# Kernel optimization log

Hardware: AMD Instinct MI355X
Metric: run time of the kernel (lower is better)

## Reference

```python
import math
import jax, jax.numpy as jnp
import numpy as np

OLEN = 512
RATIO = 0.5
DROP_P = 0.2


def _gat(x, src, dst, W, a_s, a_d, b):
    """PyG GATConv (heads=1, concat=True, add_self_loops=True, neg_slope=0.2)."""
    n = x.shape[0]
    loops = jnp.arange(n, dtype=src.dtype)
    s = jnp.concatenate([src, loops])  # [E+N] source nodes
    d = jnp.concatenate([dst, loops])  # [E+N] destination nodes
    h = x @ W                           # [N, H]
    alpha_s = h @ a_s                   # [N]
    alpha_d = h @ a_d                   # [N]
    e = jax.nn.leaky_relu(alpha_s[s] + alpha_d[d], 0.2)  # [E+N]
    # segment softmax over destination neighborhoods
    m = jax.ops.segment_max(e, d, num_segments=n)
    ee = jnp.exp(e - m[d])
    denom = jax.ops.segment_sum(ee, d, num_segments=n)
    alpha = ee / denom[d]
    out = jax.ops.segment_sum(alpha[:, None] * h[s], d, num_segments=n)
    return out + b


def _forward(x, src, dst, W1, a_src1, a_dst1, b1, W2, a_src2, a_dst2, b2,
             W3, a_src3, a_dst3, b3, W_rel, W_root, b_pool):
    N, E = x.shape[0], src.shape[0]
    key = jax.random.key(42)
    h = x
    for i, (W, a_s, a_d, b) in enumerate([(W1, a_src1, a_dst1, b1),
                                          (W2, a_src2, a_dst2, b2),
                                          (W3, a_src3, a_dst3, b3)]):
        h = jax.nn.relu(_gat(h, src, dst, W, a_s, a_d, b))
        keep = jax.random.bernoulli(jax.random.fold_in(key, i), 1.0 - DROP_P, h.shape)
        h = jnp.where(keep, h / (1.0 - DROP_P), 0.0)  # F.dropout(training=True)

    # SAGPooling(GraphConv score, ratio=0.5, tanh) repeated until n <= 512.
    # Node counts are static per iteration (k = ceil(0.5*n)); edge arrays keep
    # fixed size E with a validity mask (edges dropped when an endpoint is pooled away).
    cur_src, cur_dst = src, dst
    emask = jnp.ones((E,), dtype=h.dtype)
    n = N
    while True:
        agg = jax.ops.segment_sum(h[cur_src] * emask[:, None], cur_dst, num_segments=n)
        score = (agg @ W_rel + h @ W_root + b_pool)[:, 0]  # GraphConv(d->1), aggr='add'
        score = jnp.tanh(score)
        k = math.ceil(RATIO * n)
        top_vals, perm = jax.lax.top_k(score, k)
        h = h[perm] * top_vals[:, None]
        inv = jnp.full((n,), -1, dtype=cur_src.dtype).at[perm].set(
            jnp.arange(k, dtype=cur_src.dtype))
        ns, nd = inv[cur_src], inv[cur_dst]
        valid = (ns >= 0) & (nd >= 0)
        emask = emask * valid.astype(emask.dtype)
        cur_src = jnp.where(valid, ns, 0)
        cur_dst = jnp.where(valid, nd, 0)
        n = k
        if n <= OLEN:
            break

    out = jnp.zeros((OLEN, h.shape[1]), h.dtype).at[:n].set(h)
    return out


def setup_inputs() -> dict:
    key = jax.random.key(0)
    ks = jax.random.split(key, 20)
    N, E, IDIM, HDIM = 50000, 800000, 128, 200
    inp = {
        "x": jax.random.normal(ks[0], (N, IDIM), jnp.float32),
        "src": jax.random.randint(ks[1], (E,), 0, N, jnp.int32),
        "dst": jax.random.randint(ks[2], (E,), 0, N, jnp.int32),
    }
    def w(k, shape, fan_in):
        return jax.random.normal(k, shape, jnp.float32) / np.sqrt(fan_in).astype(np.float32)
    inp["W1"] = w(ks[3], (IDIM, HDIM), IDIM)
    inp["a_src1"] = w(ks[4], (HDIM,), HDIM)
    inp["a_dst1"] = w(ks[5], (HDIM,), HDIM)
    inp["b1"] = jnp.zeros((HDIM,), jnp.float32)
    inp["W2"] = w(ks[6], (HDIM, HDIM), HDIM)
    inp["a_src2"] = w(ks[7], (HDIM,), HDIM)
    inp["a_dst2"] = w(ks[8], (HDIM,), HDIM)
    inp["b2"] = jnp.zeros((HDIM,), jnp.float32)
    inp["W3"] = w(ks[9], (HDIM, HDIM), HDIM)
    inp["a_src3"] = w(ks[10], (HDIM,), HDIM)
    inp["a_dst3"] = w(ks[11], (HDIM,), HDIM)
    inp["b3"] = jnp.zeros((HDIM,), jnp.float32)
    inp["W_rel"] = w(ks[12], (HDIM, 1), HDIM)
    inp["W_root"] = w(ks[13], (HDIM, 1), HDIM)
    inp["b_pool"] = jnp.zeros((1,), jnp.float32)
    return inp


def reference(x, src, dst, W1, a_src1, a_dst1, b1, W2, a_src2, a_dst2, b2,
              W3, a_src3, a_dst3, b3, W_rel, W_root, b_pool):
    return _forward(x, src, dst, W1, a_src1, a_dst1, b1, W2, a_src2, a_dst2, b2,
                    W3, a_src3, a_dst3, b3, W_rel, W_root, b_pool)
```

## Files before the change

kernel.cpp:

```cpp
#include <hip/hip_runtime.h>
#include <cstdint>
#include <cstddef>


__host__ __device__ inline void tf_round(uint32_t &x0, uint32_t &x1, int r) {
  x0 += x1;
  x1 = (x1 << r) | (x1 >> (32 - r));
  x1 ^= x0;
}

__host__ __device__ inline void threefry2x32(uint32_t k0, uint32_t k1,
                                             uint32_t &x0, uint32_t &x1) {
  uint32_t ks2 = k0 ^ k1 ^ 0x1BD11BDAu;
  x0 += k0; x1 += k1;
  tf_round(x0, x1, 13); tf_round(x0, x1, 15); tf_round(x0, x1, 26); tf_round(x0, x1, 6);
  x0 += k1; x1 += ks2 + 1u;
  tf_round(x0, x1, 17); tf_round(x0, x1, 29); tf_round(x0, x1, 16); tf_round(x0, x1, 24);
  x0 += ks2; x1 += k0 + 2u;
  tf_round(x0, x1, 13); tf_round(x0, x1, 15); tf_round(x0, x1, 26); tf_round(x0, x1, 6);
  x0 += k0; x1 += k1 + 3u;
  tf_round(x0, x1, 17); tf_round(x0, x1, 29); tf_round(x0, x1, 16); tf_round(x0, x1, 24);
  x0 += k1; x1 += ks2 + 4u;
  tf_round(x0, x1, 13); tf_round(x0, x1, 15); tf_round(x0, x1, 26); tf_round(x0, x1, 6);
  x0 += ks2; x1 += k0 + 5u;
}

__global__ __launch_bounds__(256) void gemm200_k(
    const float* __restrict__ A, const float* __restrict__ B,
    float* __restrict__ C, int M, int K) {
  __shared__ float As[128 * 9];
  __shared__ __align__(16) float Bs[8][208];
  int tid = threadIdx.x;
  int m0 = blockIdx.x * 128;
  int r = tid >> 2;
  int colBase = (tid & 3) * 52;
  int nq = (colBase == 156) ? 11 : 13;
  float acc0[52], acc1[52];
#pragma unroll
  for (int q = 0; q < 52; q++) { acc0[q] = 0.f; acc1[q] = 0.f; }

  int arow = tid >> 1;
  int ac = (tid & 1) * 4;
  int gmA = m0 + arow;
  const float* Aptr = A + (size_t)gmA * K + ac;
  int bk0 = tid / 50, bc0 = (tid - bk0 * 50) * 4;
  int t2 = tid + 256;
  int bk1 = t2 / 50, bc1 = (t2 - bk1 * 50) * 4;
  bool hasB1 = (t2 < 400);

  float4 va = make_float4(0.f, 0.f, 0.f, 0.f);
  if (gmA < M) va = *(const float4*)(Aptr);
  float4 vb0 = *(const float4*)(B + (size_t)bk0 * 200 + bc0);
  float4 vb1 = make_float4(0.f, 0.f, 0.f, 0.f);
  if (hasB1) vb1 = *(const float4*)(B + (size_t)bk1 * 200 + bc1);

  for (int k0 = 0; k0 < K; k0 += 8) {
    As[arow * 9 + ac + 0] = va.x;
    As[arow * 9 + ac + 1] = va.y;
    As[arow * 9 + ac + 2] = va.z;
    As[arow * 9 + ac + 3] = va.w;
    *(float4*)(&Bs[bk0][bc0]) = vb0;
    if (hasB1) *(float4*)(&Bs[bk1][bc1]) = vb1;
    __syncthreads();
    int kn = k0 + 8;
    if (kn < K) {
      if (gmA < M) va = *(const float4*)(Aptr + kn);
      vb0 = *(const float4*)(B + (size_t)(kn + bk0) * 200 + bc0);
      if (hasB1) vb1 = *(const float4*)(B + (size_t)(kn + bk1) * 200 + bc1);
    }
#pragma unroll
    for (int kk = 0; kk < 8; kk++) {
      float a0 = As[r * 9 + kk];
      float a1 = As[(r + 64) * 9 + kk];
#pragma unroll
      for (int q = 0; q < 13; q++) {
        float4 b = *(const float4*)(&Bs[kk][colBase + 4 * q]);
        acc0[4 * q + 0] += a0 * b.x; acc0[4 * q + 1] += a0 * b.y;
        acc0[4 * q + 2] += a0 * b.z; acc0[4 * q + 3] += a0 * b.w;
        acc1[4 * q + 0] += a1 * b.x; acc1[4 * q + 1] += a1 * b.y;
        acc1[4 * q + 2] += a1 * b.z; acc1[4 * q + 3] += a1 * b.w;
      }
    }
    __syncthreads();
  }
  int gm0 = m0 + r, gm1 = m0 + r + 64;
#pragma unroll
  for (int q = 0; q < 13; q++) {
    if (q < nq) {
      int col = colBase + 4 * q;
      float4 v0 = make_float4(acc0[4 * q + 0], acc0[4 * q + 1],
                              acc0[4 * q + 2], acc0[4 * q + 3]);
      float4 v1 = make_float4(acc1[4 * q + 0], acc1[4 * q + 1],
                              acc1[4 * q + 2], acc1[4 * q + 3]);
      if (gm0 < M) *(float4*)(C + (size_t)gm0 * 200 + col) = v0;
      if (gm1 < M) *(float4*)(C + (size_t)gm1 * 200 + col) = v1;
    }
  }
}

__global__ __launch_bounds__(256) void dual_dot_k(
    const float* __restrict__ H, const float* __restrict__ v1,
    const float* __restrict__ v2, float* __restrict__ o1,
    float* __restrict__ o2, int n) {
  int wave = blockIdx.x * 4 + (threadIdx.x >> 6);
  int lane = threadIdx.x & 63;
  if (wave >= n) return;
  const float* row = H + (size_t)wave * 200;
  float s1 = 0.f, s2 = 0.f;
  for (int d = lane; d < 200; d += 64) {
    float h = row[d];
    s1 += h * v1[d];
    s2 += h * v2[d];
  }
  for (int off = 32; off; off >>= 1) {
    s1 += __shfl_down(s1, off);
    s2 += __shfl_down(s2, off);
  }
  if (lane == 0) { o1[wave] = s1; o2[wave] = s2; }
}

__global__ __launch_bounds__(256) void indeg_k(const int* __restrict__ dst,
                                               int* __restrict__ cnt, int E) {
  int e = blockIdx.x * 256 + threadIdx.x;
  if (e < E) atomicAdd(&cnt[dst[e]], 1);
}

__global__ __launch_bounds__(256) void scan_k(const int* __restrict__ cnt,
                                              int* __restrict__ rowptr, int N) {
  __shared__ int psum[256];
  int t = threadIdx.x;
  int CH = (N + 255) / 256;
  int beg = t * CH, end = min(beg + CH, N);
  if (beg > N) { beg = N; }
  int s = 0;
  for (int i = beg; i < end; i++) s += cnt[i];
  psum[t] = s;
  __syncthreads();
  if (t == 0) {
    int run = 0;
    for (int i = 0; i < 256; i++) { int v = psum[i]; psum[i] = run; run += v; }
  }
  __syncthreads();
  int run = psum[t];
  for (int i = beg; i < end; i++) { rowptr[i] = run; run += cnt[i]; }
  if (end == N && beg <= N) rowptr[N] = run;
}

__global__ __launch_bounds__(256) void cpyint_k(const int* __restrict__ a,
                                                int* __restrict__ b, int n) {
  int i = blockIdx.x * 256 + threadIdx.x;
  if (i < n) b[i] = a[i];
}

__global__ __launch_bounds__(256) void place_k(const int* __restrict__ dst,
                                               int* __restrict__ curs,
                                               int* __restrict__ csr, int E) {
  int e = blockIdx.x * 256 + threadIdx.x;
  if (e >= E) return;
  int pos = atomicAdd(&curs[dst[e]], 1);
  csr[pos] = e;
}

__global__ __launch_bounds__(256) void sortrow_k(const int* __restrict__ rowptr,
                                                 int* __restrict__ csr, int N) {
  int d = blockIdx.x * 256 + threadIdx.x;
  if (d >= N) return;
  int b = rowptr[d], e2 = rowptr[d + 1];
  for (int i = b + 1; i < e2; i++) {
    int v = csr[i];
    int j = i - 1;
    while (j >= b && csr[j] > v) { csr[j + 1] = csr[j]; j--; }
    csr[j + 1] = v;
  }
}

__device__ inline float dec_ord(unsigned enc) {
  unsigned b = (enc & 0x80000000u) ? (enc ^ 0x80000000u) : ~enc;
  return __uint_as_float(b);
}

__global__ __launch_bounds__(256) void edge_max_k(
    const int* __restrict__ src, const int* __restrict__ dst,
    const float* __restrict__ as_, const float* __restrict__ ad_,
    unsigned* __restrict__ menc, int E, int N) {
  int j = blockIdx.x * 256 + threadIdx.x;
  if (j >= E + N) return;
  int s, d;
  if (j < E) { s = src[j]; d = dst[j]; } else { s = j - E; d = s; }
  float v = as_[s] + ad_[d];
  float ev = (v >= 0.f) ? v : 0.2f * v;
  unsigned b = __float_as_uint(ev);
  unsigned enc = (b & 0x80000000u) ? ~b : (b | 0x80000000u);
  atomicMax(&menc[d], enc);
}

__global__ __launch_bounds__(256) void ee_k(
    const int* __restrict__ src, const int* __restrict__ dst,
    const float* __restrict__ as_, const float* __restrict__ ad_,
    const unsigned* __restrict__ menc, float* __restrict__ ee, int E, int N) {
  int j = blockIdx.x * 256 + threadIdx.x;
  if (j >= E + N) return;
  int s, d;
  if (j < E) { s = src[j]; d = dst[j]; } else { s = j - E; d = s; }
  float v = as_[s] + ad_[d];
  float ev = (v >= 0.f) ? v : 0.2f * v;
  ee[j] = expf(ev - dec_ord(menc[d]));
}

__global__ __launch_bounds__(256) void den_k(const int* __restrict__ rowptr,
                                             const int* __restrict__ csr,
                                             const float* __restrict__ ee,
                                             float* __restrict__ den, int E, int N) {
  int d = blockIdx.x * 256 + threadIdx.x;
  if (d >= N) return;
  float s = 0.f;
  int b = rowptr[d], e2 = rowptr[d + 1];
  for (int i = b; i < e2; i++) s = __fadd_rn(s, ee[csr[i]]);
  s = __fadd_rn(s, ee[E + d]);
  den[d] = s;
}

__global__ __launch_bounds__(256) void alpha_k(const int* __restrict__ dst,
                                               const float* __restrict__ den,
                                               float* __restrict__ ee, int E, int N) {
  int j = blockIdx.x * 256 + threadIdx.x;
  if (j >= E + N) return;
  int d = (j < E) ? dst[j] : (j - E);
  ee[j] = ee[j] / den[d];
}

#define GLD(s) (*(const float4*)(Hl + (size_t)(s) * 200))
#define ACC(W_, H_)                                    \
  acc.x = __fadd_rn(acc.x, __fmul_rn((W_), (H_).x));   \
  acc.y = __fadd_rn(acc.y, __fmul_rn((W_), (H_).y));   \
  acc.z = __fadd_rn(acc.z, __fmul_rn((W_), (H_).z));   \
  acc.w = __fadd_rn(acc.w, __fmul_rn((W_), (H_).w));

__global__ __launch_bounds__(256) void gat_out_k(
    const int* __restrict__ rowptr, const int* __restrict__ csr,
    const int* __restrict__ src, const float* __restrict__ alpha,
    const float* __restrict__ HW, float* __restrict__ OUT, int E, int N) {
  int node = blockIdx.x * 4 + (threadIdx.x >> 6);
  int lane = threadIdx.x & 63;
  if (node >= N || lane >= 50) return;
  int b = rowptr[node];
  int deg = rowptr[node + 1] - b;
  int cnt = deg + 1;
  const float* __restrict__ Hl = HW + 4 * lane;

  auto fS = [&](int t, int &s, float &w) {
    if (t < deg) {
      int e = csr[b + t];
      s = src[e];
      w = alpha[e];
    } else if (t == deg) {
      s = node;
      w = alpha[E + node];
    } else {
      s = node;
      w = 0.f;
    }
  };

  int sa, sb, sc, sd, se, sf, sn;
  float w0, w1, w2, w3, w4, w5, wn;
  fS(0, sa, w0); fS(1, sb, w1); fS(2, sc, w2); fS(3, sd, w3);
  float4 h0 = GLD(sa), h1 = GLD(sb), h2 = GLD(sc), h3 = GLD(sd);
  fS(4, se, w4);
  fS(5, sf, w5);

  float4 acc = make_float4(0.f, 0.f, 0.f, 0.f);
  for (int t = 0; t < cnt; t++) {
    float4 h4 = GLD(se);
    fS(t + 6, sn, wn);
    ACC(w0, h0);
    h0 = h1; h1 = h2; h2 = h3; h3 = h4;
    w0 = w1; w1 = w2; w2 = w3; w3 = w4; w4 = w5; w5 = wn;
    se = sf; sf = sn;
  }
  *(float4*)(OUT + (size_t)node * 200 + 4 * lane) = acc;
}

__global__ __launch_bounds__(256) void epi_k(float* __restrict__ H,
                                             const float* __restrict__ bias,
                                             uint32_t k0, uint32_t k1, int total) {
  int t = blockIdx.x * 256 + threadIdx.x;
  if (t >= total) return;
  uint32_t x0 = 0u, x1 = (uint32_t)t;
  threefry2x32(k0, k1, x0, x1);
  uint32_t bits = x0 ^ x1;
  float u = __uint_as_float((bits >> 9) | 0x3f800000u) - 1.0f;
  int col = t % 200;
  float v = H[t] + bias[col];
  v = fmaxf(v, 0.f);
  H[t] = (u < 0.8f) ? (v / 0.8f) : 0.f;
}

__global__ __launch_bounds__(256) void einit_k(
    const int* __restrict__ src, const int* __restrict__ dst,
    int* __restrict__ cs, int* __restrict__ cd, int* __restrict__ orig,
    int E, int N) {
  int e = blockIdx.x * 256 + threadIdx.x;
  if (e < E) { cs[e] = src[e]; cd[e] = dst[e]; }
  if (e < N) orig[e] = e;
}

__global__ __launch_bounds__(256) void pool_agg_k(
    const int* __restrict__ rowptr, const int* __restrict__ csr,
    const int* __restrict__ csrc, const int* __restrict__ orig,
    const float* __restrict__ H, float* __restrict__ AGG, int n) {
  int node = blockIdx.x * 4 + (threadIdx.x >> 6);
  int lane = threadIdx.x & 63;
  if (node >= n || lane >= 50) return;
  int o = orig[node];
  int b = rowptr[o];
  int deg = rowptr[o + 1] - b;
  const float* __restrict__ Hl = H + 4 * lane;

  auto fS = [&](int t, int &s, float &w) {
    if (t < deg) {
      int e = csr[b + t];
      int sv = csrc[e];
      s = (sv >= 0) ? sv : 0;
      w = (sv >= 0) ? 1.f : 0.f;
    } else {
      s = 0;
      w = 0.f;
    }
  };

  int sa, sb, sc, sd, se, sf, sn;
  float w0, w1, w2, w3, w4, w5, wn;
  fS(0, sa, w0); fS(1, sb, w1); fS(2, sc, w2); fS(3, sd, w3);
  float4 h0 = GLD(sa), h1 = GLD(sb), h2 = GLD(sc), h3 = GLD(sd);
  fS(4, se, w4);
  fS(5, sf, w5);

  float4 acc = make_float4(0.f, 0.f, 0.f, 0.f);
  for (int t = 0; t < deg; t++) {
    float4 h4 = GLD(se);
    fS(t + 6, sn, wn);
    ACC(w0, h0);
    h0 = h1; h1 = h2; h2 = h3; h3 = h4;
    w0 = w1; w1 = w2; w2 = w3; w3 = w4; w4 = w5; w5 = wn;
    se = sf; sf = sn;
  }
  *(float4*)(AGG + (size_t)node * 200 + 4 * lane) = acc;
}
#undef GLD
#undef ACC

__global__ __launch_bounds__(256) void score2_k(
    const float* __restrict__ AGG, const float* __restrict__ H,
    const float* __restrict__ wrel, const float* __restrict__ wroot,
    const float* __restrict__ bp, float* __restrict__ score, int n) {
  int node = blockIdx.x * 4 + (threadIdx.x >> 6);
  int lane = threadIdx.x & 63;
  if (node >= n) return;
  const float* arow = AGG + (size_t)node * 200;
  const float* hrow = H + (size_t)node * 200;
  float s1 = 0.f, s2 = 0.f;
  for (int d = lane; d < 200; d += 64) {
    s1 += arow[d] * wrel[d];
    s2 += hrow[d] * wroot[d];
  }
  for (int off = 32; off; off >>= 1) {
    s1 += __shfl_down(s1, off);
    s2 += __shfl_down(s2, off);
  }
  if (lane == 0) score[node] = tanhf((s1 + s2) + bp[0]);
}


__global__ __launch_bounds__(256) void rhenc_k(const float* __restrict__ score,
                                               unsigned* __restrict__ keyA,
                                               int* __restrict__ payA,
                                               int* __restrict__ counts,
                                               int n, int NB) {
  __shared__ int hist[256];
  hist[threadIdx.x] = 0;
  __syncthreads();
  int i = blockIdx.x * 256 + threadIdx.x;
  if (i < n) {
    unsigned b = __float_as_uint(score[i]);
    if (b == 0x80000000u) b = 0u;
    unsigned enc = (b & 0x80000000u) ? ~b : (b | 0x80000000u);
    unsigned key = ~enc;
    keyA[i] = key;
    payA[i] = i;
    atomicAdd(&hist[key & 255u], 1);
  }
  __syncthreads();
  counts[threadIdx.x * NB + blockIdx.x] = hist[threadIdx.x];
}

__global__ __launch_bounds__(256) void rscan_k(int* __restrict__ counts,
                                               int* __restrict__ base, int NB) {
  __shared__ int tot[256];
  int t = threadIdx.x;
  int s = 0;
  for (int b = 0; b < NB; b++) s += counts[t * NB + b];
  tot[t] = s;
  __syncthreads();
  if (t == 0) {
    int run = 0;
    for (int i = 0; i < 256; i++) { int v = tot[i]; tot[i] = run; run += v; }
  }
  __syncthreads();
  int run = tot[t];
  for (int b = 0; b < NB; b++) {
    int c = counts[t * NB + b];
    base[t * NB + b] = run;
    run += c;
    counts[t * NB + b] = 0;
  }
}

__global__ __launch_bounds__(256) void rscatter_k(
    const unsigned* __restrict__ keyIn, const int* __restrict__ payIn,
    const int* __restrict__ base, unsigned* __restrict__ keyOut,
    int* __restrict__ payOut, int* __restrict__ countsNext,
    int n, int NB, int shift) {
  __shared__ int dig[256];
  int t = threadIdx.x;
  int i = blockIdx.x * 256 + t;
  unsigned k = 0u;
  int p = 0, d = -1;
  if (i < n) {
    k = keyIn[i];
    p = payIn[i];
    d = (int)((k >> shift) & 255u);
  }
  dig[t] = d;
  __syncthreads();
  if (i < n) {
    int local = 0;
    for (int j = 0; j < t; j++) local += (dig[j] == d) ? 1 : 0;
    int pos = base[d * NB + blockIdx.x] + local;
    keyOut[pos] = k;
    payOut[pos] = p;
    int nd = (int)((k >> (shift + 8)) & 255u);
    atomicAdd(&countsNext[nd * NB + (pos >> 8)], 1);
  }
}

__global__ __launch_bounds__(256) void rscatterF_k(
    const unsigned* __restrict__ keyIn, const int* __restrict__ payIn,
    const int* __restrict__ base, const int* __restrict__ oin,
    int* __restrict__ oout, int* __restrict__ perm, int* __restrict__ inv,
    int n, int NB, int k) {
  __shared__ int dig[256];
  int t = threadIdx.x;
  int i = blockIdx.x * 256 + t;
  int p = 0, d = -1;
  if (i < n) {
    p = payIn[i];
    d = (int)((keyIn[i] >> 24) & 255u);
  }
  dig[t] = d;
  __syncthreads();
  if (i < n) {
    int local = 0;
    for (int j = 0; j < t; j++) local += (dig[j] == d) ? 1 : 0;
    int pos = base[d * NB + blockIdx.x] + local;
    if (pos < k) { perm[pos] = p; inv[p] = pos; oout[pos] = oin[p]; }
    else inv[p] = -1;
  }
}

__global__ __launch_bounds__(256) void gather_k(
    const float* __restrict__ H, const int* __restrict__ perm,
    const float* __restrict__ score, float* __restrict__ Ho, int k) {
  int r = blockIdx.x;
  int d = threadIdx.x;
  int p = perm[r];
  float s = score[p];
  if (d < 200) Ho[(size_t)r * 200 + d] = __fmul_rn(H[(size_t)p * 200 + d], s);
}

__global__ __launch_bounds__(256) void remap_k(int* __restrict__ cs,
                                               int* __restrict__ cd,
                                               const int* __restrict__ inv, int E) {
  int e = blockIdx.x * 256 + threadIdx.x;
  if (e >= E) return;
  int a = cs[e];
  if (a < 0) return;
  int na = inv[a], nb = inv[cd[e]];
  bool valid = (na >= 0) && (nb >= 0);
  cs[e] = valid ? na : -1;
  cd[e] = valid ? nb : -1;
}

__global__ __launch_bounds__(256) void out_copy_k(const float* __restrict__ h,
                                                  float* __restrict__ out, int cnt) {
  int t = blockIdx.x * 256 + threadIdx.x;
  if (t < cnt) out[t] = h[t];
}

extern "C" void kernel_launch(void* const* d_in, const int* in_sizes, int n_in,
                              void* d_out, int out_size, void* d_ws, size_t ws_size,
                              hipStream_t stream) {
  const int ID = 128, HD = 200;
  const int N = in_sizes[0] / ID;
  const int E = in_sizes[1];
  const int ET = E + N;
  const int total = N * HD;

  const float* x = (const float*)d_in[0];
  const int* src = (const int*)d_in[1];
  const int* dst = (const int*)d_in[2];
  const float* W[3]   = {(const float*)d_in[3], (const float*)d_in[7], (const float*)d_in[11]};
  const float* asv[3] = {(const float*)d_in[4], (const float*)d_in[8], (const float*)d_in[12]};
  const float* adv[3] = {(const float*)d_in[5], (const float*)d_in[9], (const float*)d_in[13]};
  const float* bv[3]  = {(const float*)d_in[6], (const float*)d_in[10], (const float*)d_in[14]};
  const float* Wrel  = (const float*)d_in[15];
  const float* Wroot = (const float*)d_in[16];
  const float* bpool = (const float*)d_in[17];

  char* ws = (char*)d_ws;
  float*    bufA  = (float*)(ws + 0);
  float*    bufB  = (float*)(ws + 40000000);
  float*    as_   = (float*)(ws + 80000000);
  float*    ad_   = (float*)(ws + 80200000);
  float*    ee_   = (float*)(ws + 80400000);
  unsigned* menc  = (unsigned*)(ws + 83800000);
  float*    den   = (float*)(ws + 84000000);
  float*    score = (float*)(ws + 84200000);
  int*      rank_ = (int*)(ws + 84400000);
  int*      perm_ = (int*)(ws + 84600000);
  int*      inv_  = (int*)(ws + 84800000);
  int*      origA = (int*)(ws + 85000000);
  int*      origB = (int*)(ws + 85200000);
  int*      rowptr= (int*)(ws + 85400000);
  int*      curs  = (int*)(ws + 85650000);
  int*      csr   = (int*)(ws + 85850000);
  int*      csrc  = (int*)(ws + 89050000);
  int*      cdst  = (int*)(ws + 92250000);

  char* rx = ws + 80400000;
  unsigned* keyA   = (unsigned*)(rx + 0 * 262144);
  unsigned* keyB   = (unsigned*)(rx + 1 * 262144);
  int*      payA   = (int*)(rx + 2 * 262144);
  int*      payB   = (int*)(rx + 3 * 262144);
  int*      rcounts= (int*)(rx + 4 * 262144);
  int*      rbase  = (int*)(rx + 5 * 262144);

  uint32_t fk0[3], fk1[3];
  for (int i = 0; i < 3; i++) {
    uint32_t a = 0u, b = (uint32_t)i;
    threefry2x32(0u, 42u, a, b);
    fk0[i] = a; fk1[i] = b;
  }

  const int B256 = 256;
  hipMemsetAsync(rank_, 0, (size_t)N * 4, stream);
  indeg_k<<<(E + 255) / 256, B256, 0, stream>>>(dst, rank_, E);
  scan_k<<<1, B256, 0, stream>>>(rank_, rowptr, N);
  cpyint_k<<<(N + 255) / 256, B256, 0, stream>>>(rowptr, curs, N);
  place_k<<<(E + 255) / 256, B256, 0, stream>>>(dst, curs, csr, E);
  sortrow_k<<<(N + 255) / 256, B256, 0, stream>>>(rowptr, csr, N);

  for (int i = 0; i < 3; i++) {
    const float* in = (i == 0) ? x : bufB;
    int K = (i == 0) ? ID : HD;
    gemm200_k<<<(N + 127) / 128, B256, 0, stream>>>(in, W[i], bufA, N, K);
    dual_dot_k<<<(N + 3) / 4, B256, 0, stream>>>(bufA, asv[i], adv[i], as_, ad_, N);
    hipMemsetAsync(menc, 0, (size_t)N * 4, stream);
    edge_max_k<<<(ET + 255) / 256, B256, 0, stream>>>(src, dst, as_, ad_, menc, E, N);
    ee_k<<<(ET + 255) / 256, B256, 0, stream>>>(src, dst, as_, ad_, menc, ee_, E, N);
    den_k<<<(N + 255) / 256, B256, 0, stream>>>(rowptr, csr, ee_, den, E, N);
    alpha_k<<<(ET + 255) / 256, B256, 0, stream>>>(dst, den, ee_, E, N);
    gat_out_k<<<(N + 3) / 4, B256, 0, stream>>>(rowptr, csr, src, ee_, bufA, bufB, E, N);
    epi_k<<<(total + 255) / 256, B256, 0, stream>>>(bufB, bv[i], fk0[i], fk1[i], total);
  }

  einit_k<<<(E + 255) / 256, B256, 0, stream>>>(src, dst, csrc, cdst, origA, E, N);
  float* hcur = bufB;
  float* hnext = bufA;
  int* ocur = origA;
  int* onext = origB;
  int n = N;
  while (true) {
    int k = (n + 1) / 2;
    int NB = (n + 255) / 256;
    pool_agg_k<<<(n + 3) / 4, B256, 0, stream>>>(rowptr, csr, csrc, ocur, hcur, hnext, n);
    score2_k<<<(n + 3) / 4, B256, 0, stream>>>(hnext, hcur, Wrel, Wroot, bpool, score, n);
    rhenc_k<<<NB, B256, 0, stream>>>(score, keyA, payA, rcounts, n, NB);
    rscan_k<<<1, B256, 0, stream>>>(rcounts, rbase, NB);
    rscatter_k<<<NB, B256, 0, stream>>>(keyA, payA, rbase, keyB, payB, rcounts, n, NB, 0);
    rscan_k<<<1, B256, 0, stream>>>(rcounts, rbase, NB);
    rscatter_k<<<NB, B256, 0, stream>>>(keyB, payB, rbase, keyA, payA, rcounts, n, NB, 8);
    rscan_k<<<1, B256, 0, stream>>>(rcounts, rbase, NB);
    rscatter_k<<<NB, B256, 0, stream>>>(keyA, payA, rbase, keyB, payB, rcounts, n, NB, 16);
    rscan_k<<<1, B256, 0, stream>>>(rcounts, rbase, NB);
    rscatterF_k<<<NB, B256, 0, stream>>>(keyB, payB, rbase, ocur, onext, perm_, inv_,
                                         n, NB, k);
    gather_k<<<k, B256, 0, stream>>>(hcur, perm_, score, hnext, k);
    remap_k<<<(E + 255) / 256, B256, 0, stream>>>(csrc, cdst, inv_, E);
    { float* t = hcur; hcur = hnext; hnext = t; }
    { int* t = ocur; ocur = onext; onext = t; }
    n = k;
    if (n <= 512) break;
  }

  hipMemsetAsync(d_out, 0, (size_t)out_size * 4, stream);
  out_copy_k<<<(n * HD + 255) / 256, B256, 0, stream>>>(hcur, (float*)d_out, n * HD);
}
```

Before: 2.988 ms.

## Fuse GAT softmax stages into CSR-ordered packed edges and fuse pooling score

Replaces the separate per-edge exp, per-node denominator and alpha-normalisation kernels with one per-destination kernel. It computes exp values in CSR order and stores (src, ee) pairs packed contiguously, so gat_out_k reads them sequentially and divides by the denominator inline. Pooling aggregation and score computation are merged, with the aggregate held in shared memory instead of a global buffer. This removes two launches and scattered gathers per GAT layer plus one launch and a global round-trip per pooling step. In exchange the softmax work is one thread per node, so load is imbalanced across high-degree nodes, and the packed buffers alias existing workspace regions.

Result: faster. 2.843 ms (-4.8%).

```diff
diff --git a/kernel.cpp b/kernel.cpp
--- a/kernel.cpp
+++ b/kernel.cpp
@@ -194,39 +194,33 @@
   atomicMax(&menc[d], enc);
 }
 
-__global__ __launch_bounds__(256) void ee_k(
-    const int* __restrict__ src, const int* __restrict__ dst,
-    const float* __restrict__ as_, const float* __restrict__ ad_,
-    const unsigned* __restrict__ menc, float* __restrict__ ee, int E, int N) {
-  int j = blockIdx.x * 256 + threadIdx.x;
-  if (j >= E + N) return;
-  int s, d;
-  if (j < E) { s = src[j]; d = dst[j]; } else { s = j - E; d = s; }
-  float v = as_[s] + ad_[d];
-  float ev = (v >= 0.f) ? v : 0.2f * v;
-  ee[j] = expf(ev - dec_ord(menc[d]));
-}
-
-__global__ __launch_bounds__(256) void den_k(const int* __restrict__ rowptr,
-                                             const int* __restrict__ csr,
-                                             const float* __restrict__ ee,
-                                             float* __restrict__ den, int E, int N) {
+__global__ __launch_bounds__(256) void eeden_k(
+    const int* __restrict__ rowptr, const int* __restrict__ csr,
+    const int* __restrict__ src, const float* __restrict__ as_,
+    const float* __restrict__ ad_, const unsigned* __restrict__ menc,
+    int2* __restrict__ pk, float* __restrict__ eeS, float* __restrict__ den,
+    int N) {
   int d = blockIdx.x * 256 + threadIdx.x;
   if (d >= N) return;
+  float m = dec_ord(menc[d]);
+  float adv = ad_[d];
+  int b = rowptr[d], e2 = rowptr[d + 1];
   float s = 0.f;
-  int b = rowptr[d], e2 = rowptr[d + 1];
-  for (int i = b; i < e2; i++) s = __fadd_rn(s, ee[csr[i]]);
-  s = __fadd_rn(s, ee[E + d]);
+  for (int i = b; i < e2; i++) {
+    int e = csr[i];
+    int sv = src[e];
+    float v = as_[sv] + adv;
+    float ev = (v >= 0.f) ? v : 0.2f * v;
+    float ee = expf(ev - m);
+    pk[i] = make_int2(sv, __float_as_int(ee));
+    s = __fadd_rn(s, ee);
+  }
+  float vS = as_[d] + adv;
+  float evS = (vS >= 0.f) ? vS : 0.2f * vS;
+  float eS = expf(evS - m);
+  eeS[d] = eS;
+  s = __fadd_rn(s, eS);
   den[d] = s;
-}
-
-__global__ __launch_bounds__(256) void alpha_k(const int* __restrict__ dst,
-                                               const float* __restrict__ den,
-                                               float* __restrict__ ee, int E, int N) {
-  int j = blockIdx.x * 256 + threadIdx.x;
-  if (j >= E + N) return;
-  int d = (j < E) ? dst[j] : (j - E);
-  ee[j] = ee[j] / den[d];
 }
 
 #define GLD(s) (*(const float4*)(Hl + (size_t)(s) * 200))
@@ -237,25 +231,26 @@
   acc.w = __fadd_rn(acc.w, __fmul_rn((W_), (H_).w));
 
 __global__ __launch_bounds__(256) void gat_out_k(
-    const int* __restrict__ rowptr, const int* __restrict__ csr,
-    const int* __restrict__ src, const float* __restrict__ alpha,
-    const float* __restrict__ HW, float* __restrict__ OUT, int E, int N) {
+    const int* __restrict__ rowptr, const int2* __restrict__ pk,
+    const float* __restrict__ eeS, const float* __restrict__ den,
+    const float* __restrict__ HW, float* __restrict__ OUT, int N) {
   int node = blockIdx.x * 4 + (threadIdx.x >> 6);
   int lane = threadIdx.x & 63;
   if (node >= N || lane >= 50) return;
   int b = rowptr[node];
   int deg = rowptr[node + 1] - b;
   int cnt = deg + 1;
+  float dn = den[node];
   const float* __restrict__ Hl = HW + 4 * lane;
 
   auto fS = [&](int t, int &s, float &w) {
     if (t < deg) {
-      int e = csr[b + t];
-      s = src[e];
-      w = alpha[e];
+      int2 p = pk[b + t];
+      s = p.x;
+      w = __fdiv_rn(__int_as_float(p.y), dn);
     } else if (t == deg) {
       s = node;
-      w = alpha[E + node];
+      w = __fdiv_rn(eeS[node], dn);
     } else {
       s = node;
       w = 0.f;
@@ -308,56 +303,56 @@
 __global__ __launch_bounds__(256) void pool_agg_k(
     const int* __restrict__ rowptr, const int* __restrict__ csr,
     const int* __restrict__ csrc, const int* __restrict__ orig,
-    const float* __restrict__ H, float* __restrict__ AGG, int n) {
-  int node = blockIdx.x * 4 + (threadIdx.x >> 6);
+    const float* __restrict__ H, const float* __restrict__ wrel,
+    const float* __restrict__ wroot, const float* __restrict__ bp,
+    float* __restrict__ score, int n) {
+  __shared__ float sagg[4][200];
+  int wv = threadIdx.x >> 6;
+  int node = blockIdx.x * 4 + wv;
   int lane = threadIdx.x & 63;
-  if (node >= n || lane >= 50) return;
+  if (node >= n) return;
   int o = orig[node];
   int b = rowptr[o];
   int deg = rowptr[o + 1] - b;
-  const float* __restrict__ Hl = H + 4 * lane;
-
-  auto fS = [&](int t, int &s, float &w) {
-    if (t < deg) {
-      int e = csr[b + t];
-      int sv = csrc[e];
-      s = (sv >= 0) ? sv : 0;
-      w = (sv >= 0) ? 1.f : 0.f;
-    } else {
-      s = 0;
-      w = 0.f;
+
+  if (lane < 50) {
+    const float* __restrict__ Hl = H + 4 * lane;
+    auto fS = [&](int t, int &s, float &w) {
+      if (t < deg) {
+        int e = csr[b + t];
+        int sv = csrc[e];
+        s = (sv >= 0) ? sv : 0;
+        w = (sv >= 0) ? 1.f : 0.f;
+      } else {
+        s = 0;
+        w = 0.f;
+      }
+    };
+
+    int sa, sb, sc, sd, se, sf, sn;
+    float w0, w1, w2, w3, w4, w5, wn;
+    fS(0, sa, w0); fS(1, sb, w1); fS(2, sc, w2); fS(3, sd, w3);
+    float4 h0 = GLD(sa), h1 = GLD(sb), h2 = GLD(sc), h3 = GLD(sd);
+    fS(4, se, w4);
+    fS(5, sf, w5);
+
+    float4 acc = make_float4(0.f, 0.f, 0.f, 0.f);
+    for (int t = 0; t < deg; t++) {
+      float4 h4 = GLD(se);
+      fS(t + 6, sn, wn);
+      ACC(w0, h0);
+      h0 = h1; h1 = h2; h2 = h3; h3 = h4;
+      w0 = w1; w1 = w2; w2 = w3; w3 = w4; w4 = w5; w5 = wn;
+      se = sf; sf = sn;
     }
-  };
-
-  int sa, sb, sc, sd, se, sf, sn;
-  float w0, w1, w2, w3, w4, w5, wn;
-  fS(0, sa, w0); fS(1, sb, w1); fS(2, sc, w2); fS(3, sd, w3);
-  float4 h0 = GLD(sa), h1 = GLD(sb), h2 = GLD(sc), h3 = GLD(sd);
-  fS(4, se, w4);
-  fS(5, sf, w5);
-
-  float4 acc = make_float4(0.f, 0.f, 0.f, 0.f);
-  for (int t = 0; t < deg; t++) {
-    float4 h4 = GLD(se);
-    fS(t + 6, sn, wn);
-    ACC(w0, h0);
-    h0 = h1; h1 = h2; h2 = h3; h3 = h4;
-    w0 = w1; w1 = w2; w2 = w3; w3 = w4; w4 = w5; w5 = wn;
-    se = sf; sf = sn;
-  }
-  *(float4*)(AGG + (size_t)node * 200 + 4 * lane) = acc;
-}
-#undef GLD
-#undef ACC
-
-__global__ __launch_bounds__(256) void score2_k(
-    const float* __restrict__ AGG, const float* __restrict__ H,
-    const float* __restrict__ wrel, const float* __restrict__ wroot,
-    const float* __restrict__ bp, float* __restrict__ score, int n) {
-  int node = blockIdx.x * 4 + (threadIdx.x >> 6);
-  int lane = threadIdx.x & 63;
-  if (node >= n) return;
-  const float* arow = AGG + (size_t)node * 200;
+    sagg[wv][4 * lane + 0] = acc.x;
+    sagg[wv][4 * lane + 1] = acc.y;
+    sagg[wv][4 * lane + 2] = acc.z;
+    sagg[wv][4 * lane + 3] = acc.w;
+  }
+  __threadfence_block();
+
+  const float* arow = sagg[wv];
   const float* hrow = H + (size_t)node * 200;
   float s1 = 0.f, s2 = 0.f;
   for (int d = lane; d < 200; d += 64) {
@@ -370,6 +365,8 @@
   }
   if (lane == 0) score[node] = tanhf((s1 + s2) + bp[0]);
 }
+#undef GLD
+#undef ACC
 
 
 __global__ __launch_bounds__(256) void rhenc_k(const float* __restrict__ score,
@@ -537,6 +534,9 @@
   int*      csrc  = (int*)(ws + 89050000);
   int*      cdst  = (int*)(ws + 92250000);
 
+  int2* pk = (int2*)(ws + 89050000);
+  float* eeS = (float*)(ws + 80400000);
+
   char* rx = ws + 80400000;
   unsigned* keyA   = (unsigned*)(rx + 0 * 262144);
   unsigned* keyB   = (unsigned*)(rx + 1 * 262144);
@@ -567,10 +567,9 @@
     dual_dot_k<<<(N + 3) / 4, B256, 0, stream>>>(bufA, asv[i], adv[i], as_, ad_, N);
     hipMemsetAsync(menc, 0, (size_t)N * 4, stream);
     edge_max_k<<<(ET + 255) / 256, B256, 0, stream>>>(src, dst, as_, ad_, menc, E, N);
-    ee_k<<<(ET + 255) / 256, B256, 0, stream>>>(src, dst, as_, ad_, menc, ee_, E, N);
-    den_k<<<(N + 255) / 256, B256, 0, stream>>>(rowptr, csr, ee_, den, E, N);
-    alpha_k<<<(ET + 255) / 256, B256, 0, stream>>>(dst, den, ee_, E, N);
-    gat_out_k<<<(N + 3) / 4, B256, 0, stream>>>(rowptr, csr, src, ee_, bufA, bufB, E, N);
+    eeden_k<<<(N + 255) / 256, B256, 0, stream>>>(rowptr, csr, src, as_, ad_, menc,
+                                                  pk, eeS, den, N);
+    gat_out_k<<<(N + 3) / 4, B256, 0, stream>>>(rowptr, pk, eeS, den, bufA, bufB, N);
     epi_k<<<(total + 255) / 256, B256, 0, stream>>>(bufB, bv[i], fk0[i], fk1[i], total);
   }
 
@@ -583,8 +582,8 @@
   while (true) {
     int k = (n + 1) / 2;
     int NB = (n + 255) / 256;
-    pool_agg_k<<<(n + 3) / 4, B256, 0, stream>>>(rowptr, csr, csrc, ocur, hcur, hnext, n);
-    score2_k<<<(n + 3) / 4, B256, 0, stream>>>(hnext, hcur, Wrel, Wroot, bpool, score, n);
+    pool_agg_k<<<(n + 3) / 4, B256, 0, stream>>>(rowptr, csr, csrc, ocur, hcur,
+                                                 Wrel, Wroot, bpool, score, n);
     rhenc_k<<<NB, B256, 0, stream>>>(score, keyA, payA, rcounts, n, NB);
     rscan_k<<<1, B256, 0, stream>>>(rcounts, rbase, NB);
     rscatter_k<<<NB, B256, 0, stream>>>(keyA, payA, rbase, keyB, payB, rcounts, n, NB, 0);
```
